# Kernel tuning notes

Measured on AMD Instinct MI355X. Metric: run time of the kernel, lower is better.

Reference implementation:

```python
import jax, jax.numpy as jnp
import numpy as np

HIDDEN, KEY_DIM, VALUE_DIM = 1024, 1024, 1024
BATCH, SEQ = 8, 2048


def setup_inputs() -> dict:
    key = jax.random.key(0)
    ks = jax.random.split(key, 9)
    s = lambda fan_in: 1.0 / np.sqrt(fan_in)
    return {
        "y_all": jax.random.normal(ks[0], (BATCH, SEQ, HIDDEN), dtype=jnp.float32),
        # torch nn.Linear weights stored as (in, out) for x @ W + b
        "Wq": jax.random.uniform(ks[1], (HIDDEN, KEY_DIM), jnp.float32, -s(HIDDEN), s(HIDDEN)),
        "bq": jax.random.uniform(ks[2], (KEY_DIM,), jnp.float32, -s(HIDDEN), s(HIDDEN)),
        "Wk": jax.random.uniform(ks[3], (HIDDEN, KEY_DIM), jnp.float32, -s(HIDDEN), s(HIDDEN)),
        "bk": jax.random.uniform(ks[4], (KEY_DIM,), jnp.float32, -s(HIDDEN), s(HIDDEN)),
        "Wv": jax.random.uniform(ks[5], (HIDDEN, VALUE_DIM), jnp.float32, -s(HIDDEN), s(HIDDEN)),
        "bv": jax.random.uniform(ks[6], (VALUE_DIM,), jnp.float32, -s(HIDDEN), s(HIDDEN)),
        "Wo": jax.random.uniform(ks[7], (VALUE_DIM, HIDDEN), jnp.float32, -s(VALUE_DIM), s(VALUE_DIM)),
        "bo": jax.random.uniform(ks[8], (HIDDEN,), jnp.float32, -s(VALUE_DIM), s(VALUE_DIM)),
    }


def reference(y_all, Wq, bq, Wk, bk, Wv, bv, Wo, bo):
    # Original loops over t, each step attending last hidden state to the full
    # prefix. Equivalent to a single causal-masked attention pass.
    B, T, H = y_all.shape
    dk = Wq.shape[1]
    q = (y_all @ Wq + bq) / jnp.sqrt(jnp.asarray(dk, y_all.dtype))  # [B,T,dk]
    k = y_all @ Wk + bk                                              # [B,T,dk]
    v = y_all @ Wv + bv                                              # [B,T,dv]
    scores = jnp.einsum("bid,bjd->bij", q, k)                        # [B,T,T]
    causal = jnp.tril(jnp.ones((T, T), dtype=bool))                  # j <= i
    scores = jnp.where(causal, scores, -jnp.inf)
    weights = jax.nn.softmax(scores, axis=-1)
    ctx = jnp.einsum("bij,bjd->bid", weights, v)                     # [B,T,dv]
    return ctx @ Wo + bo                                             # [B,T,H]
```

## Files before the change

kernel.cpp:

```cpp
#include <hip/hip_runtime.h>

typedef __attribute__((ext_vector_type(8))) __bf16 bf16x8;
typedef __attribute__((ext_vector_type(4))) float f32x4;
typedef __attribute__((ext_vector_type(4))) float f4;
typedef __attribute__((ext_vector_type(4))) unsigned short ushort4_t;

__device__ inline void gload16(const void* g, void* l) {
  __builtin_amdgcn_global_load_lds(
      (const __attribute__((address_space(1))) unsigned int*)g,
      (__attribute__((address_space(3))) unsigned int*)l, 16, 0, 0);
}

#define FENCE asm volatile("" ::: "memory")

__global__ __launch_bounds__(256) void prep_k(
    const float* __restrict__ y,
    const float* __restrict__ Wq, const float* __restrict__ Wk,
    const float* __restrict__ Wv, const float* __restrict__ Wo,
    const float* __restrict__ bq, const float* __restrict__ bk,
    const float* __restrict__ bv,
    __bf16* __restrict__ Xb, __bf16* __restrict__ Wt, float* __restrict__ bqkv) {
  __shared__ float tile[32][33];
  const int bid = blockIdx.x, t = threadIdx.x;
  if (bid < 2048) {
    for (int i = bid * 256 + t; i < 2097152; i += 524288) {
      f4 a = ((const f4*)y)[2 * (long long)i];
      f4 b = ((const f4*)y)[2 * (long long)i + 1];
      bf16x8 o;
#pragma unroll
      for (int e = 0; e < 4; e++) { o[e] = (__bf16)a[e]; o[e + 4] = (__bf16)b[e]; }
      ((bf16x8*)Xb)[i] = o;
    }
  } else if (bid < 6144) {
    const int idx = bid - 2048;
    const int z = idx >> 10, rem = idx & 1023;
    const int bx = rem & 31, by = rem >> 5;
    const float* W = (z == 0) ? Wq : (z == 1) ? Wk : (z == 2) ? Wv : Wo;
    __bf16* O = Wt + (long long)z * 1048576;
    const int tx = t & 31, ty = t >> 5;
    const int n0 = bx * 32, k0 = by * 32;
#pragma unroll
    for (int i = 0; i < 4; i++)
      tile[ty + i * 8][tx] = W[(long long)(k0 + ty + i * 8) * 1024 + n0 + tx];
    __syncthreads();
#pragma unroll
    for (int i = 0; i < 4; i++)
      O[(long long)(n0 + ty + i * 8) * 1024 + k0 + tx] = (__bf16)tile[tx][ty + i * 8];
  } else {
    const int i = (bid - 6144) * 256 + t;
    if (i < 3072) {
      const float* src = (i < 1024) ? bq : (i < 2048) ? bk : bv;
      bqkv[i] = src[i & 1023];
    }
  }
}


#define LOADA(BASE, MIB)                                                       \
  _Pragma("unroll") for (int mi = 0; mi < 4; mi++)                             \
      _Pragma("unroll") for (int kh = 0; kh < 2; kh++) {                       \
    int row = ((MIB) + mi) * 16 + ln15;                                        \
    int pb = (row * 128 + (kh * 32 + kq * 8) * 2) ^ ((row & 7) << 4);          \
    a[mi][kh] = *(const bf16x8*)((BASE) + pb);                                 \
  }

#define LOADB(BASE, NIB)                                                       \
  _Pragma("unroll") for (int ni = 0; ni < 2; ni++)                             \
      _Pragma("unroll") for (int kh = 0; kh < 2; kh++) {                       \
    int row = brow0 + ((NIB) + ni) * 16 + ln15;                                \
    int pb = (row * 128 + (kh * 32 + kq * 8) * 2) ^ ((row & 7) << 4);          \
    b[(NIB) + ni][kh] = *(const bf16x8*)((BASE) + pb);                         \
  }

#define MFMAQ(MI0, NI0)                                                        \
  _Pragma("unroll") for (int mi = 0; mi < 4; mi++)                             \
      _Pragma("unroll") for (int ni = 0; ni < 2; ni++)                         \
          _Pragma("unroll") for (int kh = 0; kh < 2; kh++)                     \
              acc[(MI0) + mi][(NI0) + ni] =                                    \
      __builtin_amdgcn_mfma_f32_16x16x32_bf16(a[mi][kh], b[(NI0) + ni][kh],    \
                                              acc[(MI0) + mi][(NI0) + ni], 0, 0, 0);

#define BARW                                           \
  FENCE;                                               \
  __builtin_amdgcn_s_barrier();                        \
  FENCE;                                               \
  __builtin_amdgcn_s_setprio(1);

#define ENDP                                           \
  __builtin_amdgcn_s_setprio(0);                       \
  FENCE;                                               \
  __builtin_amdgcn_s_barrier();                        \
  FENCE;

#define ENDPB                                          \
  __builtin_amdgcn_s_setprio(0);                       \
  asm volatile("s_waitcnt vmcnt(8)" ::: "memory");     \
  __builtin_amdgcn_s_barrier();                        \
  FENCE;

template <int OUT, int SWZ>
__global__ __launch_bounds__(512, 2) void gemm8(
    const __bf16* __restrict__ A0, int lda, long long sAz,
    const __bf16* __restrict__ B0, int ldb, long long sBz,
    void* __restrict__ C0v, int ldc, long long sCz,
    const float* __restrict__ bias0, int sBiasZ,
    float scale_z0, int k_tiles_base, int k_tiles_per_br) {
  int br, bc, z;
  {
    const int lin = (blockIdx.z * gridDim.y + blockIdx.y) * gridDim.x + blockIdx.x;
    if (SWZ == 1) {
      const int q = lin & 7, c = lin >> 3;
      br = q * 8 + (c & 7);
      const int rest = c >> 3;
      const int nby = gridDim.y;
      bc = rest % nby;
      z = rest / nby;
    } else {
      const int nbx = gridDim.x, nby = gridDim.y;
      const int nwg = nbx * nby * gridDim.z;
      const int cpx = nwg >> 3;
      const int swz = (lin & 7) * cpx + (lin >> 3);
      br = swz % nbx;
      const int tmp = swz / nbx;
      bc = tmp % nby;
      z = tmp / nby;
    }
  }
  const int kt = k_tiles_base + k_tiles_per_br * br;

  __shared__ __align__(16) __bf16 lds[81920];

  const int t = threadIdx.x, w = t >> 6, lane = t & 63;
  const int wm = w >> 2, wn = w & 3;
  const int ln15 = lane & 15, kq = lane >> 4;
  const int bh = wn >> 1, brow0 = (wn & 1) * 64;

  const __bf16* A = A0 + (long long)z * sAz + (long long)br * 256 * lda;
  const __bf16* B = B0 + (long long)z * sBz + (long long)bc * 256 * ldb;

  int r0s[2], c0s[2];
#pragma unroll
  for (int i = 0; i < 2; i++) {
    int o = i * 8192 + t * 16;
    int lo = o ^ (((o >> 7) & 7) << 4);
    r0s[i] = lo >> 7;
    c0s[i] = (lo & 127) >> 1;
  }
  const __bf16 *sA0[2], *sA1[2], *sB0[2], *sB1[2];
#pragma unroll
  for (int i = 0; i < 2; i++) {
    sA0[i] = A + (long long)r0s[i] * lda + c0s[i];
    sA1[i] = A + (long long)(r0s[i] + 128) * lda + c0s[i];
    sB0[i] = B + (long long)r0s[i] * ldb + c0s[i];
    sB1[i] = B + (long long)(r0s[i] + 128) * ldb + c0s[i];
  }

  auto stg = [&](const __bf16* const* src, __bf16* lbase, int g) {
    int kc = g < kt ? g : kt - 1;
#pragma unroll
    for (int i = 0; i < 2; i++)
      gload16(src[i] + kc * 64, lbase + i * 4096 + w * 512);
  };

  f32x4 acc[8][4] = {};
  bf16x8 a[4][2], b[4][2];

  stg(sA0, lds, 0);
  stg(sA1, lds + 8192, 0);
  stg(sB0, lds + 49152, 0);
  stg(sB1, lds + 49152 + 8192, 0);
  stg(sA0, lds + 16384, 1);
  stg(sA1, lds + 16384 + 8192, 1);
  stg(sB0, lds + 65536, 1);
  stg(sB1, lds + 65536 + 8192, 1);
  asm volatile("s_waitcnt vmcnt(8)" ::: "memory");
  __builtin_amdgcn_s_barrier();
  FENCE;

  int ap = 0, ad = 2;
  for (int kk = 0; kk < kt; kk++) {
    __bf16* Ab = lds + ap * 16384;
    __bf16* Bb = lds + 49152 + (kk & 1) * 16384;
    __bf16* Ad = lds + ad * 16384;
    __bf16* Bd = Bb;
    const char* Aw = (const char*)(Ab + wm * 8192);
    const char* Bw = (const char*)(Bb + bh * 8192);
    LOADA(Aw, 0) LOADB(Bw, 0)
    stg(sA0, Ad, kk + 2);
    BARW MFMAQ(0, 0) ENDP
    LOADB(Bw, 2)
    stg(sA1, Ad + 8192, kk + 2);
    BARW MFMAQ(0, 2) ENDP
    LOADA(Aw, 4)
    stg(sB0, Bd, kk + 2);
    BARW MFMAQ(4, 2) ENDP
    stg(sB1, Bd + 8192, kk + 2);
    BARW MFMAQ(4, 0) ENDPB
    ap = (ap == 2) ? 0 : ap + 1;
    ad = (ad == 2) ? 0 : ad + 1;
  }

  {
    const int row0 = br * 256 + wm * 128 + kq * 4;
    const int col0 = bc * 256 + wn * 64 + ln15;
    const float scale = (z == 0) ? scale_z0 : 1.0f;
    const float* bias = bias0 ? (bias0 + (long long)z * sBiasZ) : nullptr;
#pragma unroll
    for (int mi = 0; mi < 8; mi++) {
#pragma unroll
      for (int ni = 0; ni < 4; ni++) {
        const int rr = row0 + mi * 16;
        const int cc = col0 + ni * 16;
        const float bb = bias ? bias[cc] : 0.0f;
#pragma unroll
        for (int j = 0; j < 4; j++) {
          float v = (acc[mi][ni][j] + bb) * scale;
          long long off = (long long)z * sCz + (long long)(rr + j) * ldc + cc;
          if (OUT == 1)
            ((float*)C0v)[off] = v;
          else
            ((__bf16*)C0v)[off] = (__bf16)v;
        }
      }
    }
  }
}

template <int OUT, int SWZ>
__global__ __launch_bounds__(512, 4) void gemm2w(
    const __bf16* __restrict__ A0, int lda, long long sAz,
    const __bf16* __restrict__ B0, int ldb, long long sBz,
    void* __restrict__ C0v, int ldc, long long sCz,
    const float* __restrict__ bias0, int sBiasZ,
    float scale_z0, int k_tiles_base, int k_tiles_per_br,
    __bf16* __restrict__ vt_out) {
  int br, bc, z;
  {
    const int lin = (blockIdx.z * gridDim.y + blockIdx.y) * gridDim.x + blockIdx.x;
    if (SWZ == 4) {
      z = lin & 7;
      const int r = (lin >> 3) & 7;
      bc = (lin >> 6) & 3;
      const int half = lin >> 8;
      br = half ? (7 - r) : (8 + r);
    } else if (SWZ == 5) {
      z = lin & 7;
      const int c = lin >> 3;
      int m = (int)((sqrtf((float)(4 * c + 1)) - 1.0f) * 0.5f);
      if (c < m * (m + 1)) m--;
      if (c >= (m + 1) * (m + 2)) m++;
      const int r = c - m * (m + 1);
      if (r >= m + 1) { br = 2 * m + 1; bc = r - (m + 1); }
      else { br = 2 * m; bc = r; }
    } else {
      const int q = lin & 7, c = lin >> 3;
      br = q * 16 + (c & 15);
      const int rest = c >> 4;
      const int nby = gridDim.y;
      bc = rest % nby;
      z = rest / nby;
    }
  }
  const int kt = k_tiles_base + k_tiles_per_br * br;

  __shared__ __align__(16) __bf16 lds[36864];

  const int t = threadIdx.x, w = t >> 6, lane = t & 63;
  const int wm = w >> 2, wn = w & 3;
  const int ln15 = lane & 15, kq = lane >> 4;

  const __bf16* A = A0 + (long long)z * sAz + (long long)br * 128 * lda;
  const __bf16* B = B0 + (long long)z * sBz + (long long)bc * 256 * ldb;

  const __bf16* sA;
  const __bf16* sB[2];
  {
    int o = t * 16;
    int lo = o ^ (((o >> 7) & 3) << 4);
    sA = A + (long long)(lo >> 6) * lda + ((lo & 63) >> 1);
  }
#pragma unroll
  for (int i = 0; i < 2; i++) {
    int o = i * 8192 + t * 16;
    int lo = o ^ (((o >> 7) & 3) << 4);
    sB[i] = B + (long long)(lo >> 6) * ldb + ((lo & 63) >> 1);
  }

  auto stgA = [&](int buf, int g) {
    int kc = g < kt ? g : kt - 1;
    gload16(sA + kc * 32, lds + buf * 4096 + w * 512);
  };
  auto stgB = [&](int buf, int g) {
    int kc = g < kt ? g : kt - 1;
#pragma unroll
    for (int i = 0; i < 2; i++)
      gload16(sB[i] + kc * 32, lds + 12288 + buf * 8192 + i * 4096 + w * 512);
  };

  f32x4 acc[4][4] = {};
  bf16x8 a[4], b[4];

  stgA(0, 0); stgB(0, 0);
  stgA(1, 1); stgB(1, 1);
  asm volatile("s_waitcnt vmcnt(3)" ::: "memory");
  __builtin_amdgcn_s_barrier();
  FENCE;

  int cb = 0, db = 2;
  for (int kk = 0; kk < kt; kk++) {
    const char* Ab = (const char*)(lds + cb * 4096);
    const char* Bb = (const char*)(lds + 12288 + cb * 8192);
#pragma unroll
    for (int mi = 0; mi < 4; mi++) {
      int row = wm * 64 + mi * 16 + ln15;
      int pb = (row * 64 + kq * 16) ^ (((row >> 1) & 3) << 4);
      a[mi] = *(const bf16x8*)(Ab + pb);
    }
#pragma unroll
    for (int ni = 0; ni < 4; ni++) {
      int row = wn * 64 + ni * 16 + ln15;
      int pb = (row * 64 + kq * 16) ^ (((row >> 1) & 3) << 4);
      b[ni] = *(const bf16x8*)(Bb + pb);
    }
    stgA(db, kk + 2);
    stgB(db, kk + 2);
    FENCE;
    __builtin_amdgcn_s_barrier();
    FENCE;
    __builtin_amdgcn_s_setprio(1);
#pragma unroll
    for (int mi = 0; mi < 4; mi++)
#pragma unroll
      for (int ni = 0; ni < 4; ni++)
        acc[mi][ni] = __builtin_amdgcn_mfma_f32_16x16x32_bf16(
            a[mi], b[ni], acc[mi][ni], 0, 0, 0);
    __builtin_amdgcn_s_setprio(0);
    asm volatile("s_waitcnt vmcnt(3)" ::: "memory");
    __builtin_amdgcn_s_barrier();
    FENCE;
    cb = (cb == 2) ? 0 : cb + 1;
    db = (db == 2) ? 0 : db + 1;
  }
  asm volatile("s_waitcnt vmcnt(0)" ::: "memory");

  if (OUT == 2 && z == 2) {
    __syncthreads();
    char* lb = (char*)lds;
#pragma unroll
    for (int mi = 0; mi < 4; mi++) {
#pragma unroll
      for (int ni = 0; ni < 4; ni++) {
        const int d = wn * 64 + ni * 16 + ln15;
        const int tl = wm * 64 + kq * 4 + mi * 16;
        const float bb = bias0[2048 + bc * 256 + d];
        ushort4_t p;
#pragma unroll
        for (int j = 0; j < 4; j++) {
          union { __bf16 h; unsigned short u; } cv;
          cv.h = (__bf16)(acc[mi][ni][j] + bb);
          p[j] = cv.u;
        }
        int byte = (d * 256 + tl * 2) ^ ((d & 7) << 4);
        *(ushort4_t*)(lb + byte) = p;
      }
    }
    __syncthreads();
    const int bz = br >> 4;
    const int t0 = (br & 15) * 128;
    __bf16* vbase = vt_out + (long long)bz * 2097152 +
                    (long long)(bc * 256) * 2048 + t0;
#pragma unroll
    for (int it = 0; it < 8; it++) {
      int idx = it * 512 + t;
      int d = idx >> 4, tc = idx & 15;
      int byte = (d * 256 + tc * 16) ^ ((d & 7) << 4);
      bf16x8 vv = *(const bf16x8*)(lb + byte);
      *(bf16x8*)(vbase + (long long)d * 2048 + tc * 8) = vv;
    }
  } else {
    const int row0 = br * 128 + wm * 64 + kq * 4;
    const int col0 = bc * 256 + wn * 64 + ln15;
    const float scale = (z == 0) ? scale_z0 : 1.0f;
    const float* bias = bias0 ? (bias0 + (long long)z * sBiasZ) : nullptr;
#pragma unroll
    for (int mi = 0; mi < 4; mi++) {
#pragma unroll
      for (int ni = 0; ni < 4; ni++) {
        const int rr = row0 + mi * 16;
        const int cc = col0 + ni * 16;
        const float bb = bias ? bias[cc] : 0.0f;
#pragma unroll
        for (int j = 0; j < 4; j++) {
          float v = (acc[mi][ni][j] + bb) * scale;
          long long off = (long long)z * sCz + (long long)(rr + j) * ldc + cc;
          if (OUT == 1)
            ((float*)C0v)[off] = v;
          else
            ((__bf16*)C0v)[off] = (__bf16)v;
        }
      }
    }
  }
}

__global__ __launch_bounds__(256) void softmax_rows(__bf16* __restrict__ S) {
  const int row = blockIdx.x;
  const int i = row & 2047;
  __bf16* s = S + (long long)row * 2048;
  const int Lpad = (i + 128) & ~127;
  const int t = threadIdx.x;
  const int j0 = t * 8;
  const int wid = t >> 6, lane = t & 63;
  const bool active = j0 < Lpad;

  float v[8];
  float mymax = -3.0e38f;
  if (active) {
    bf16x8 x = *(const bf16x8*)(s + j0);
#pragma unroll
    for (int e = 0; e < 8; e++) {
      float f = (float)x[e];
      v[e] = ((j0 + e) <= i) ? f : -3.0e38f;
      mymax = fmaxf(mymax, v[e]);
    }
  }
  float mw = mymax;
#pragma unroll
  for (int o = 32; o >= 1; o >>= 1) mw = fmaxf(mw, __shfl_xor(mw, o));
  __shared__ float redm[4];
  __shared__ float reds[4];
  if (lane == 0) redm[wid] = mw;
  __syncthreads();
  const float m = fmaxf(fmaxf(redm[0], redm[1]), fmaxf(redm[2], redm[3]));

  float e8[8];
  float mysum = 0.0f;
  if (active) {
#pragma unroll
    for (int e = 0; e < 8; e++) {
      float ev = ((j0 + e) <= i) ? __expf(v[e] - m) : 0.0f;
      e8[e] = ev;
      mysum += ev;
    }
  } else {
#pragma unroll
    for (int e = 0; e < 8; e++) e8[e] = 0.0f;
  }
  float sw = mysum;
#pragma unroll
  for (int o = 32; o >= 1; o >>= 1) sw += __shfl_xor(sw, o);
  if (lane == 0) reds[wid] = sw;
  __syncthreads();
  const float l = reds[0] + reds[1] + reds[2] + reds[3];
  const float rl = 1.0f / l;
  if (active) {
    bf16x8 o;
#pragma unroll
    for (int e = 0; e < 8; e++) o[e] = (__bf16)(e8[e] * rl);
    *(bf16x8*)(s + j0) = o;
  }
}

extern "C" void kernel_launch(void* const* d_in, const int* in_sizes, int n_in,
                              void* d_out, int out_size, void* d_ws, size_t ws_size,
                              hipStream_t stream) {
  const float* y  = (const float*)d_in[0];
  const float* Wq = (const float*)d_in[1];
  const float* bq = (const float*)d_in[2];
  const float* Wk = (const float*)d_in[3];
  const float* bk = (const float*)d_in[4];
  const float* Wv = (const float*)d_in[5];
  const float* bv = (const float*)d_in[6];
  const float* Wo = (const float*)d_in[7];
  const float* bo = (const float*)d_in[8];

  char* ws = (char*)d_ws;
  __bf16* Xb   = (__bf16*)(ws + 0);
  __bf16* Wt   = (__bf16*)(ws + 33554432);
  float*  bqkv = (float*)(ws + 41943040);
  __bf16* Qb   = (__bf16*)(ws + 41955328);
  __bf16* Kb   = (__bf16*)(ws + 75509760);
  __bf16* Vt   = (__bf16*)(ws + 109064192);
  __bf16* Sb   = (__bf16*)(ws + 142618624);
  __bf16* ctx  = (__bf16*)(ws + 0);

  if (ws_size < 209727488u) return;

  prep_k<<<6156, 256, 0, stream>>>(y, Wq, Wk, Wv, Wo, bq, bk, bv, Xb, Wt, bqkv);

  gemm2w<2, 0><<<dim3(128, 4, 3), 512, 0, stream>>>(
      Xb, 1024, 0LL, Wt, 1024, 1048576LL,
      Qb, 1024, 16777216LL, bqkv, 1024, 0.03125f, 32, 0, Vt);

  gemm2w<0, 5><<<dim3(576, 1, 1), 512, 0, stream>>>(
      Qb, 1024, 2097152LL, Kb, 1024, 2097152LL,
      Sb, 2048, 4194304LL, nullptr, 0, 1.0f, 32, 0, nullptr);

  softmax_rows<<<16384, 256, 0, stream>>>(Sb);

  gemm2w<0, 4><<<dim3(512, 1, 1), 512, 0, stream>>>(
      Sb, 2048, 4194304LL, Vt, 2048, 2097152LL,
      ctx, 1024, 2097152LL, nullptr, 0, 1.0f, 4, 4, nullptr);

  gemm8<1, 1><<<dim3(64, 4, 1), 512, 0, stream>>>(
      ctx, 1024, 0LL, Wt + 3 * 1048576, 1024, 0LL,
      d_out, 1024, 0LL, bo, 0, 1.0f, 16, 0);
}
```

Measured before the change: 298.6 us.

## Fuse softmax into QK^T epilogue and normalize in PV epilogue

Removes the separate softmax kernel: the QK^T GEMM epilogue now writes exp(scores) with the causal mask and atomically accumulates per-row sums into unused padding columns of the score buffer, which prep_k zeroes. The PV GEMM epilogue then divides by the row sum. No max subtraction is done, which relies on the scaled scores being small enough not to overflow exp. The final output projection also switches from gemm8 to gemm2w with 128-row tiles.

```diff
diff --git a/kernel.cpp b/kernel.cpp
--- a/kernel.cpp
+++ b/kernel.cpp
@@ -19,7 +19,8 @@
     const float* __restrict__ Wv, const float* __restrict__ Wo,
     const float* __restrict__ bq, const float* __restrict__ bk,
     const float* __restrict__ bv,
-    __bf16* __restrict__ Xb, __bf16* __restrict__ Wt, float* __restrict__ bqkv) {
+    __bf16* __restrict__ Xb, __bf16* __restrict__ Wt, float* __restrict__ bqkv,
+    char* __restrict__ sb) {
   __shared__ float tile[32][33];
   const int bid = blockIdx.x, t = threadIdx.x;
   if (bid < 2048) {
@@ -46,15 +47,17 @@
 #pragma unroll
     for (int i = 0; i < 4; i++)
       O[(long long)(n0 + ty + i * 8) * 1024 + k0 + tx] = (__bf16)tile[tx][ty + i * 8];
-  } else {
+  } else if (bid < 6156) {
     const int i = (bid - 6144) * 256 + t;
     if (i < 3072) {
       const float* src = (i < 1024) ? bq : (i < 2048) ? bk : bv;
       bqkv[i] = src[i & 1023];
     }
+  } else {
+    const int gr = (bid - 6156) * 256 + t;
+    *(float*)(sb + (long long)(gr & 127) * 4096 + 2048 + (gr >> 7) * 4) = 0.0f;
   }
 }
-
 
 #define LOADA(BASE, MIB)                                                       \
   _Pragma("unroll") for (int mi = 0; mi < 4; mi++)                             \
@@ -97,134 +100,6 @@
   asm volatile("s_waitcnt vmcnt(8)" ::: "memory");     \
   __builtin_amdgcn_s_barrier();                        \
   FENCE;
-
-template <int OUT, int SWZ>
-__global__ __launch_bounds__(512, 2) void gemm8(
-    const __bf16* __restrict__ A0, int lda, long long sAz,
-    const __bf16* __restrict__ B0, int ldb, long long sBz,
-    void* __restrict__ C0v, int ldc, long long sCz,
-    const float* __restrict__ bias0, int sBiasZ,
-    float scale_z0, int k_tiles_base, int k_tiles_per_br) {
-  int br, bc, z;
-  {
-    const int lin = (blockIdx.z * gridDim.y + blockIdx.y) * gridDim.x + blockIdx.x;
-    if (SWZ == 1) {
-      const int q = lin & 7, c = lin >> 3;
-      br = q * 8 + (c & 7);
-      const int rest = c >> 3;
-      const int nby = gridDim.y;
-      bc = rest % nby;
-      z = rest / nby;
-    } else {
-      const int nbx = gridDim.x, nby = gridDim.y;
-      const int nwg = nbx * nby * gridDim.z;
-      const int cpx = nwg >> 3;
-      const int swz = (lin & 7) * cpx + (lin >> 3);
-      br = swz % nbx;
-      const int tmp = swz / nbx;
-      bc = tmp % nby;
-      z = tmp / nby;
-    }
-  }
-  const int kt = k_tiles_base + k_tiles_per_br * br;
-
-  __shared__ __align__(16) __bf16 lds[81920];
-
-  const int t = threadIdx.x, w = t >> 6, lane = t & 63;
-  const int wm = w >> 2, wn = w & 3;
-  const int ln15 = lane & 15, kq = lane >> 4;
-  const int bh = wn >> 1, brow0 = (wn & 1) * 64;
-
-  const __bf16* A = A0 + (long long)z * sAz + (long long)br * 256 * lda;
-  const __bf16* B = B0 + (long long)z * sBz + (long long)bc * 256 * ldb;
-
-  int r0s[2], c0s[2];
-#pragma unroll
-  for (int i = 0; i < 2; i++) {
-    int o = i * 8192 + t * 16;
-    int lo = o ^ (((o >> 7) & 7) << 4);
-    r0s[i] = lo >> 7;
-    c0s[i] = (lo & 127) >> 1;
-  }
-  const __bf16 *sA0[2], *sA1[2], *sB0[2], *sB1[2];
-#pragma unroll
-  for (int i = 0; i < 2; i++) {
-    sA0[i] = A + (long long)r0s[i] * lda + c0s[i];
-    sA1[i] = A + (long long)(r0s[i] + 128) * lda + c0s[i];
-    sB0[i] = B + (long long)r0s[i] * ldb + c0s[i];
-    sB1[i] = B + (long long)(r0s[i] + 128) * ldb + c0s[i];
-  }
-
-  auto stg = [&](const __bf16* const* src, __bf16* lbase, int g) {
-    int kc = g < kt ? g : kt - 1;
-#pragma unroll
-    for (int i = 0; i < 2; i++)
-      gload16(src[i] + kc * 64, lbase + i * 4096 + w * 512);
-  };
-
-  f32x4 acc[8][4] = {};
-  bf16x8 a[4][2], b[4][2];
-
-  stg(sA0, lds, 0);
-  stg(sA1, lds + 8192, 0);
-  stg(sB0, lds + 49152, 0);
-  stg(sB1, lds + 49152 + 8192, 0);
-  stg(sA0, lds + 16384, 1);
-  stg(sA1, lds + 16384 + 8192, 1);
-  stg(sB0, lds + 65536, 1);
-  stg(sB1, lds + 65536 + 8192, 1);
-  asm volatile("s_waitcnt vmcnt(8)" ::: "memory");
-  __builtin_amdgcn_s_barrier();
-  FENCE;
-
-  int ap = 0, ad = 2;
-  for (int kk = 0; kk < kt; kk++) {
-    __bf16* Ab = lds + ap * 16384;
-    __bf16* Bb = lds + 49152 + (kk & 1) * 16384;
-    __bf16* Ad = lds + ad * 16384;
-    __bf16* Bd = Bb;
-    const char* Aw = (const char*)(Ab + wm * 8192);
-    const char* Bw = (const char*)(Bb + bh * 8192);
-    LOADA(Aw, 0) LOADB(Bw, 0)
-    stg(sA0, Ad, kk + 2);
-    BARW MFMAQ(0, 0) ENDP
-    LOADB(Bw, 2)
-    stg(sA1, Ad + 8192, kk + 2);
-    BARW MFMAQ(0, 2) ENDP
-    LOADA(Aw, 4)
-    stg(sB0, Bd, kk + 2);
-    BARW MFMAQ(4, 2) ENDP
-    stg(sB1, Bd + 8192, kk + 2);
-    BARW MFMAQ(4, 0) ENDPB
-    ap = (ap == 2) ? 0 : ap + 1;
-    ad = (ad == 2) ? 0 : ad + 1;
-  }
-
-  {
-    const int row0 = br * 256 + wm * 128 + kq * 4;
-    const int col0 = bc * 256 + wn * 64 + ln15;
-    const float scale = (z == 0) ? scale_z0 : 1.0f;
-    const float* bias = bias0 ? (bias0 + (long long)z * sBiasZ) : nullptr;
-#pragma unroll
-    for (int mi = 0; mi < 8; mi++) {
-#pragma unroll
-      for (int ni = 0; ni < 4; ni++) {
-        const int rr = row0 + mi * 16;
-        const int cc = col0 + ni * 16;
-        const float bb = bias ? bias[cc] : 0.0f;
-#pragma unroll
-        for (int j = 0; j < 4; j++) {
-          float v = (acc[mi][ni][j] + bb) * scale;
-          long long off = (long long)z * sCz + (long long)(rr + j) * ldc + cc;
-          if (OUT == 1)
-            ((float*)C0v)[off] = v;
-          else
-            ((__bf16*)C0v)[off] = (__bf16)v;
-        }
-      }
-    }
-  }
-}
 
 template <int OUT, int SWZ>
 __global__ __launch_bounds__(512, 4) void gemm2w(
@@ -377,6 +252,52 @@
       bf16x8 vv = *(const bf16x8*)(lb + byte);
       *(bf16x8*)(vbase + (long long)d * 2048 + tc * 8) = vv;
     }
+  } else if (OUT == 3) {
+    char* lsb = (char*)vt_out;
+    const int row0 = br * 128 + wm * 64 + kq * 4;
+    const int col0 = bc * 256 + wn * 64 + ln15;
+#pragma unroll
+    for (int mi = 0; mi < 4; mi++) {
+#pragma unroll
+      for (int j = 0; j < 4; j++) {
+        const int rr = row0 + mi * 16 + j;
+        float psum = 0.0f;
+#pragma unroll
+        for (int ni = 0; ni < 4; ni++) {
+          const int cc = col0 + ni * 16;
+          float p = (cc <= rr) ? __expf(acc[mi][ni][j]) : 0.0f;
+          __bf16 pb = (__bf16)p;
+          ((__bf16*)C0v)[(long long)z * sCz + (long long)rr * ldc + cc] = pb;
+          psum += (float)pb;
+        }
+#pragma unroll
+        for (int o = 8; o >= 1; o >>= 1) psum += __shfl_xor(psum, o);
+        if (ln15 == 0) {
+          const int gr = z * 2048 + rr;
+          atomicAdd((float*)(lsb + (long long)(gr & 127) * 4096 + 2048 +
+                             (gr >> 7) * 4),
+                    psum);
+        }
+      }
+    }
+  } else if (OUT == 4) {
+    const int row0 = br * 128 + wm * 64 + kq * 4;
+    const int col0 = bc * 256 + wn * 64 + ln15;
+#pragma unroll
+    for (int mi = 0; mi < 4; mi++) {
+#pragma unroll
+      for (int j = 0; j < 4; j++) {
+        const int rr = row0 + mi * 16 + j;
+        const int gr = z * 2048 + rr;
+        const float rl = 1.0f / bias0[(gr & 127) * 1024 + 512 + (gr >> 7)];
+#pragma unroll
+        for (int ni = 0; ni < 4; ni++) {
+          const int cc = col0 + ni * 16;
+          ((__bf16*)C0v)[(long long)z * sCz + (long long)rr * ldc + cc] =
+              (__bf16)(acc[mi][ni][j] * rl);
+        }
+      }
+    }
   } else {
     const int row0 = br * 128 + wm * 64 + kq * 4;
     const int col0 = bc * 256 + wn * 64 + ln15;
@@ -400,64 +321,6 @@
         }
       }
     }
-  }
-}
-
-__global__ __launch_bounds__(256) void softmax_rows(__bf16* __restrict__ S) {
-  const int row = blockIdx.x;
-  const int i = row & 2047;
-  __bf16* s = S + (long long)row * 2048;
-  const int Lpad = (i + 128) & ~127;
-  const int t = threadIdx.x;
-  const int j0 = t * 8;
-  const int wid = t >> 6, lane = t & 63;
-  const bool active = j0 < Lpad;
-
-  float v[8];
-  float mymax = -3.0e38f;
-  if (active) {
-    bf16x8 x = *(const bf16x8*)(s + j0);
-#pragma unroll
-    for (int e = 0; e < 8; e++) {
-      float f = (float)x[e];
-      v[e] = ((j0 + e) <= i) ? f : -3.0e38f;
-      mymax = fmaxf(mymax, v[e]);
-    }
-  }
-  float mw = mymax;
-#pragma unroll
-  for (int o = 32; o >= 1; o >>= 1) mw = fmaxf(mw, __shfl_xor(mw, o));
-  __shared__ float redm[4];
-  __shared__ float reds[4];
-  if (lane == 0) redm[wid] = mw;
-  __syncthreads();
-  const float m = fmaxf(fmaxf(redm[0], redm[1]), fmaxf(redm[2], redm[3]));
-
-  float e8[8];
-  float mysum = 0.0f;
-  if (active) {
-#pragma unroll
-    for (int e = 0; e < 8; e++) {
-      float ev = ((j0 + e) <= i) ? __expf(v[e] - m) : 0.0f;
-      e8[e] = ev;
-      mysum += ev;
-    }
-  } else {
-#pragma unroll
-    for (int e = 0; e < 8; e++) e8[e] = 0.0f;
-  }
-  float sw = mysum;
-#pragma unroll
-  for (int o = 32; o >= 1; o >>= 1) sw += __shfl_xor(sw, o);
-  if (lane == 0) reds[wid] = sw;
-  __syncthreads();
-  const float l = reds[0] + reds[1] + reds[2] + reds[3];
-  const float rl = 1.0f / l;
-  if (active) {
-    bf16x8 o;
-#pragma unroll
-    for (int e = 0; e < 8; e++) o[e] = (__bf16)(e8[e] * rl);
-    *(bf16x8*)(s + j0) = o;
   }
 }
 
@@ -486,23 +349,22 @@
 
   if (ws_size < 209727488u) return;
 
-  prep_k<<<6156, 256, 0, stream>>>(y, Wq, Wk, Wv, Wo, bq, bk, bv, Xb, Wt, bqkv);
+  prep_k<<<6220, 256, 0, stream>>>(y, Wq, Wk, Wv, Wo, bq, bk, bv, Xb, Wt, bqkv,
+                                   (char*)Sb);
 
   gemm2w<2, 0><<<dim3(128, 4, 3), 512, 0, stream>>>(
       Xb, 1024, 0LL, Wt, 1024, 1048576LL,
       Qb, 1024, 16777216LL, bqkv, 1024, 0.03125f, 32, 0, Vt);
 
-  gemm2w<0, 5><<<dim3(576, 1, 1), 512, 0, stream>>>(
+  gemm2w<3, 5><<<dim3(576, 1, 1), 512, 0, stream>>>(
       Qb, 1024, 2097152LL, Kb, 1024, 2097152LL,
-      Sb, 2048, 4194304LL, nullptr, 0, 1.0f, 32, 0, nullptr);
-
-  softmax_rows<<<16384, 256, 0, stream>>>(Sb);
-
-  gemm2w<0, 4><<<dim3(512, 1, 1), 512, 0, stream>>>(
+      Sb, 2048, 4194304LL, nullptr, 0, 1.0f, 32, 0, Sb);
+
+  gemm2w<4, 4><<<dim3(512, 1, 1), 512, 0, stream>>>(
       Sb, 2048, 4194304LL, Vt, 2048, 2097152LL,
-      ctx, 1024, 2097152LL, nullptr, 0, 1.0f, 4, 4, nullptr);
-
-  gemm8<1, 1><<<dim3(64, 4, 1), 512, 0, stream>>>(
+      ctx, 1024, 2097152LL, (const float*)Sb, 0, 1.0f, 4, 4, nullptr);
+
+  gemm2w<1, 0><<<dim3(128, 4, 1), 512, 0, stream>>>(
       ctx, 1024, 0LL, Wt + 3 * 1048576, 1024, 0LL,
-      d_out, 1024, 0LL, bo, 0, 1.0f, 16, 0);
+      d_out, 1024, 0LL, bo, 0, 1.0f, 32, 0, nullptr);
 }
```

Result: no change. 298.7 us (+0.0%).
